# Performance work log

Hardware: AMD Instinct MI355X
Metric: run time of the kernel (lower is better)

## Reference

```python
import jax, jax.numpy as jnp
import numpy as np

EMBED = 2048
HEADS = 16
HEAD_DIM = EMBED // HEADS


def setup_inputs() -> dict:
    key = jax.random.key(0)
    k1, k2 = jax.random.split(key)
    X = jax.random.normal(k1, (2, 2048, EMBED), dtype=jnp.float32)
    W_qkv = jax.random.normal(k2, (EMBED, 3 * EMBED), dtype=jnp.float32) * (1.0 / np.sqrt(EMBED))
    b_qkv = jnp.zeros((3 * EMBED,), dtype=jnp.float32)
    return {"X": X, "W_qkv": W_qkv, "b_qkv": b_qkv}


def reference(X, W_qkv, b_qkv):
    B, S, D = X.shape
    qkv = jnp.einsum('bsd,de->bse', X, W_qkv) + b_qkv  # [B,S,3D]
    q, k, v = jnp.split(qkv, 3, axis=-1)
    # [B,S,D] -> [B,H,S,hd]
    def heads(t):
        return t.reshape(B, S, HEADS, HEAD_DIM).transpose(0, 2, 1, 3)
    q, k, v = heads(q), heads(k), heads(v)
    scale = 1.0 / np.sqrt(HEAD_DIM).astype(np.float32)
    attention_score = jnp.einsum('bhqd,bhkd->bhqk', q, k) * scale
    scores = jax.nn.softmax(attention_score, axis=-1)  # [B,H,S,S]
    attention = jnp.einsum('bhqk,bhkd->bhqd', scores, v)
    attention = attention.transpose(0, 2, 1, 3).reshape(B, S, D)
    return (attention, scores)
```

## Files before the change

### kernel.cpp

```cpp
#include <hip/hip_runtime.h>
#include <hip/hip_bf16.h>

typedef __attribute__((ext_vector_type(8))) short short8;
typedef __attribute__((ext_vector_type(4))) float floatx4;

#define SEQ 2048
#define EMB 2048
#define NH 16
#define HD 128
#define E3 6144
#define SC2 0.12751224765383853f

static __device__ __forceinline__ unsigned short f2bf(float f) {
  unsigned u = __builtin_bit_cast(unsigned, f);
  u += 0x7fffu + ((u >> 16) & 1u);
  return (unsigned short)(u >> 16);
}

__global__ void k_tw(const float* __restrict__ W, unsigned short* __restrict__ Wt) {
  __shared__ unsigned short t[32][33];
  int tx = threadIdx.x, ty = threadIdx.y;
  int e0 = blockIdx.x * 32, d0 = blockIdx.y * 32;
#pragma unroll
  for (int k = 0; k < 4; k++)
    t[ty + k * 8][tx] = f2bf(W[(long)(d0 + ty + k * 8) * E3 + e0 + tx]);
  __syncthreads();
#pragma unroll
  for (int k = 0; k < 4; k++)
    Wt[(long)(e0 + ty + k * 8) * EMB + d0 + tx] = t[tx][ty + k * 8];
}

__global__ void k_tv(const unsigned short* __restrict__ qkv, unsigned short* __restrict__ Vt) {
  __shared__ unsigned short t[32][33];
  int tx = threadIdx.x, ty = threadIdx.y;
  int z = blockIdx.z;
  int b = z >> 4, h = z & 15;
  int s0 = blockIdx.x * 32, d0 = blockIdx.y * 32;
#pragma unroll
  for (int k = 0; k < 4; k++) {
    int s = s0 + ty + k * 8;
    t[ty + k * 8][tx] = qkv[(long)(b * SEQ + s) * E3 + 2 * EMB + h * HD + d0 + tx];
  }
  __syncthreads();
#pragma unroll
  for (int k = 0; k < 4; k++) {
    int d = d0 + ty + k * 8;
    Vt[((long)z * HD + d) * SEQ + s0 + tx] = t[tx][ty + k * 8];
  }
}

template <int MODE>
__global__ __launch_bounds__(256, 2) void k_gemm(const void* __restrict__ Abase,
                                                 const unsigned short* __restrict__ Btb,
                                                 void* __restrict__ Cb,
                                                 const float* __restrict__ bias,
                                                 float scale) {
  constexpr int K = (MODE == 1) ? 128 : 2048;
  constexpr long sA = (MODE == 0) ? EMB : (MODE == 1) ? E3 : SEQ;
  constexpr long sB = (MODE == 0) ? EMB : (MODE == 1) ? E3 : SEQ;
  constexpr long sC = (MODE == 0) ? E3 : (MODE == 1) ? SEQ : EMB;
  constexpr bool AF32 = (MODE != 1);

  int z = blockIdx.z;
  long offA = 0, offB = 0, offC = 0;
  if (MODE == 1) {
    int b = z >> 4, h = z & 15;
    offA = (long)(b * SEQ) * E3 + h * HD;
    offB = (long)(b * SEQ) * E3 + EMB + h * HD;
    offC = (long)z * SEQ * SEQ;
  } else if (MODE == 2) {
    int b = z >> 4, h = z & 15;
    offA = (long)z * SEQ * SEQ;
    offB = (long)z * HD * SEQ;
    offC = (long)b * SEQ * EMB + h * HD;
  }

  __shared__ unsigned short As[128][72];
  __shared__ unsigned short Bs[128][72];

  int tid = threadIdx.x;
  int lane = tid & 63;
  int wave = tid >> 6;
  int wm = wave >> 1, wn = wave & 1;
  int quad = lane >> 4, l16 = lane & 15;
  long tM = (long)blockIdx.y * 128;
  long tN = (long)blockIdx.x * 128;

  const float* Af = (const float*)Abase;
  const unsigned short* Ab = (const unsigned short*)Abase;

  floatx4 acc[4][4] = {};

  for (int k0 = 0; k0 < K; k0 += 64) {
#pragma unroll
    for (int c = 0; c < 4; c++) {
      int id = tid + 256 * c;
      int r = id >> 3;
      int col = (id & 7) * 8;
      if (AF32) {
        const float* s = Af + offA + (tM + r) * sA + k0 + col;
        float4 f0 = *(const float4*)s;
        float4 f1 = *(const float4*)(s + 4);
        uint4 u;
        u.x = (unsigned)f2bf(f0.x) | ((unsigned)f2bf(f0.y) << 16);
        u.y = (unsigned)f2bf(f0.z) | ((unsigned)f2bf(f0.w) << 16);
        u.z = (unsigned)f2bf(f1.x) | ((unsigned)f2bf(f1.y) << 16);
        u.w = (unsigned)f2bf(f1.z) | ((unsigned)f2bf(f1.w) << 16);
        *(uint4*)&As[r][col] = u;
      } else {
        *(uint4*)&As[r][col] = *(const uint4*)(Ab + offA + (tM + r) * sA + k0 + col);
      }
      *(uint4*)&Bs[r][col] = *(const uint4*)(Btb + offB + (tN + r) * sB + k0 + col);
    }
    __syncthreads();
#pragma unroll
    for (int ks = 0; ks < 2; ks++) {
      short8 af[4], bfr[4];
#pragma unroll
      for (int i = 0; i < 4; i++)
        af[i] = *(const short8*)&As[wm * 64 + i * 16 + l16][ks * 32 + quad * 8];
#pragma unroll
      for (int j = 0; j < 4; j++)
        bfr[j] = *(const short8*)&Bs[wn * 64 + j * 16 + l16][ks * 32 + quad * 8];
#pragma unroll
      for (int i = 0; i < 4; i++)
#pragma unroll
        for (int j = 0; j < 4; j++)
          acc[i][j] = __builtin_amdgcn_mfma_f32_16x16x32_bf16(af[i], bfr[j], acc[i][j], 0, 0, 0);
    }
    __syncthreads();
  }

#pragma unroll
  for (int i = 0; i < 4; i++)
#pragma unroll
    for (int j = 0; j < 4; j++)
#pragma unroll
      for (int r = 0; r < 4; r++) {
        long row = tM + wm * 64 + i * 16 + quad * 4 + r;
        long col = tN + wn * 64 + j * 16 + l16;
        float v = acc[i][j][r];
        if (MODE == 0) {
          ((unsigned short*)Cb)[row * sC + col] = f2bf(v + bias[col]);
        } else if (MODE == 1) {
          ((float*)Cb)[offC + row * sC + col] = v * scale;
        } else {
          ((float*)Cb)[offC + row * sC + col] = v;
        }
      }
}

__global__ __launch_bounds__(256, 2) void k_attn(const unsigned short* __restrict__ qkv,
                                                 const unsigned short* __restrict__ Vt,
                                                 float* __restrict__ scores,
                                                 float* __restrict__ attn) {
  int id = blockIdx.x;
  int z = (id & 7) * 4 + ((id >> 3) >> 4);
  int qt = (id >> 3) & 15;
  int b = z >> 4, h = z & 15;

  const unsigned short* Qg = qkv + (long)b * SEQ * E3 + h * HD;
  const unsigned short* Kg = Qg + EMB;
  const unsigned short* Vg = Vt + (long)z * HD * SEQ;
  float* Sg = scores + (long)z * SEQ * SEQ + (long)qt * 128 * SEQ;
  float* Og = attn + (long)b * SEQ * EMB + (long)qt * 128 * EMB + h * HD;

  __shared__ unsigned short Kt[64][136];
  __shared__ unsigned short Vs[128][72];
  __shared__ unsigned short Ps[128][72];

  int tid = threadIdx.x;
  int lane = tid & 63, wave = tid >> 6;
  int quad = lane >> 4, l16 = lane & 15;

  short8 qf[2][4];
#pragma unroll
  for (int i = 0; i < 2; i++)
#pragma unroll
    for (int ks = 0; ks < 4; ks++)
      qf[i][ks] = *(const short8*)(Qg + (long)(qt * 128 + wave * 32 + i * 16 + l16) * E3 +
                                   ks * 32 + quad * 8);

  floatx4 oacc[2][8] = {};
  float rs[2][4] = {};

  uint4 kreg[4], vreg[4];
  auto loadK = [&](int t) {
#pragma unroll
    for (int c = 0; c < 4; c++) {
      int i2 = tid + 256 * c;
      kreg[c] = *(const uint4*)(Kg + (long)(t * 64 + (i2 >> 4)) * E3 + (i2 & 15) * 8);
    }
  };
  auto loadV = [&](int t) {
#pragma unroll
    for (int c = 0; c < 4; c++) {
      int i2 = tid + 256 * c;
      vreg[c] = *(const uint4*)(Vg + (long)(i2 >> 3) * SEQ + t * 64 + (i2 & 7) * 8);
    }
  };

  loadK(0);
  loadV(0);

  for (int t = 0; t < 32; t++) {
#pragma unroll
    for (int c = 0; c < 4; c++) {
      int i2 = tid + 256 * c;
      *(uint4*)&Kt[i2 >> 4][(i2 & 15) * 8] = kreg[c];
      *(uint4*)&Vs[i2 >> 3][(i2 & 7) * 8] = vreg[c];
    }
    __syncthreads();
    if (t < 31) { loadK(t + 1); loadV(t + 1); }

    floatx4 sacc[2][4] = {};
#pragma unroll
    for (int ks = 0; ks < 4; ks++) {
      short8 kf[4];
#pragma unroll
      for (int j = 0; j < 4; j++)
        kf[j] = *(const short8*)&Kt[j * 16 + l16][ks * 32 + quad * 8];
#pragma unroll
      for (int i = 0; i < 2; i++)
#pragma unroll
        for (int j = 0; j < 4; j++)
          sacc[i][j] = __builtin_amdgcn_mfma_f32_16x16x32_bf16(qf[i][ks], kf[j], sacc[i][j], 0, 0, 0);
    }
#pragma unroll
    for (int i = 0; i < 2; i++)
#pragma unroll
      for (int j = 0; j < 4; j++)
#pragma unroll
        for (int r = 0; r < 4; r++) {
          float e = exp2f(sacc[i][j][r] * SC2);
          rs[i][r] += e;
          Ps[wave * 32 + i * 16 + quad * 4 + r][j * 16 + l16] = f2bf(e);
        }
    __syncthreads();
#pragma unroll
    for (int ks = 0; ks < 2; ks++) {
      short8 pf[2], vf[8];
#pragma unroll
      for (int i = 0; i < 2; i++)
        pf[i] = *(const short8*)&Ps[wave * 32 + i * 16 + l16][ks * 32 + quad * 8];
#pragma unroll
      for (int j = 0; j < 8; j++)
        vf[j] = *(const short8*)&Vs[j * 16 + l16][ks * 32 + quad * 8];
#pragma unroll
      for (int i = 0; i < 2; i++)
#pragma unroll
        for (int j = 0; j < 8; j++)
          oacc[i][j] = __builtin_amdgcn_mfma_f32_16x16x32_bf16(pf[i], vf[j], oacc[i][j], 0, 0, 0);
    }
    __syncthreads();
  }

  loadK(0);

  float irs[2][4];
#pragma unroll
  for (int i = 0; i < 2; i++)
#pragma unroll
    for (int r = 0; r < 4; r++) {
      float s = rs[i][r];
      s += __shfl_xor(s, 1, 64);
      s += __shfl_xor(s, 2, 64);
      s += __shfl_xor(s, 4, 64);
      s += __shfl_xor(s, 8, 64);
      irs[i][r] = 1.0f / s;
    }

#pragma unroll
  for (int i = 0; i < 2; i++)
#pragma unroll
    for (int j = 0; j < 8; j++)
#pragma unroll
      for (int r = 0; r < 4; r++)
        Og[(long)(wave * 32 + i * 16 + quad * 4 + r) * EMB + j * 16 + l16] =
            oacc[i][j][r] * irs[i][r];

  for (int t = 0; t < 32; t++) {
#pragma unroll
    for (int c = 0; c < 4; c++) {
      int i2 = tid + 256 * c;
      *(uint4*)&Kt[i2 >> 4][(i2 & 15) * 8] = kreg[c];
    }
    __syncthreads();
    if (t < 31) loadK(t + 1);

    floatx4 sacc[2][4] = {};
#pragma unroll
    for (int ks = 0; ks < 4; ks++) {
      short8 kf[4];
#pragma unroll
      for (int j = 0; j < 4; j++)
        kf[j] = *(const short8*)&Kt[j * 16 + l16][ks * 32 + quad * 8];
#pragma unroll
      for (int i = 0; i < 2; i++)
#pragma unroll
        for (int j = 0; j < 4; j++)
          sacc[i][j] = __builtin_amdgcn_mfma_f32_16x16x32_bf16(qf[i][ks], kf[j], sacc[i][j], 0, 0, 0);
    }
#pragma unroll
    for (int i = 0; i < 2; i++)
#pragma unroll
      for (int j = 0; j < 4; j++)
#pragma unroll
        for (int r = 0; r < 4; r++)
          Sg[(long)(wave * 32 + i * 16 + quad * 4 + r) * SEQ + t * 64 + j * 16 + l16] =
              exp2f(sacc[i][j][r] * SC2) * irs[i][r];
    __syncthreads();
  }
}

extern "C" void kernel_launch(void* const* d_in, const int* in_sizes, int n_in,
                              void* d_out, int out_size, void* d_ws, size_t ws_size,
                              hipStream_t stream) {
  const float* X = (const float*)d_in[0];
  const float* W = (const float*)d_in[1];
  const float* bias = (const float*)d_in[2];
  float* out = (float*)d_out;
  float* attn = out;
  float* scores = out + (long)2 * SEQ * EMB;

  unsigned short* Wt = (unsigned short*)d_ws;
  unsigned short* qkv = Wt + (long)E3 * EMB;
  unsigned short* Vt = qkv + (long)2 * SEQ * E3;

  k_tw<<<dim3(E3 / 32, EMB / 32), dim3(32, 8), 0, stream>>>(W, Wt);
  k_gemm<0><<<dim3(E3 / 128, (2 * SEQ) / 128, 1), 256, 0, stream>>>(X, Wt, qkv, bias, 1.0f);
  k_tv<<<dim3(SEQ / 32, HD / 32, 2 * NH), dim3(32, 8), 0, stream>>>(qkv, Vt);
  k_attn<<<dim3(512), dim3(256), 0, stream>>>(qkv, Vt, scores, attn);
}
```

Baseline: 1.161 ms.

## Pre-convert X to bf16 and use direct global-to-LDS loads in projection GEMM

Adds a kernel that converts X to bf16 once, so the projection GEMM no longer converts fp32 to bf16 in every tile. The projection GEMM now fills shared memory with global_load_lds 16-byte transfers, drops the padded LDS layout, and remaps blocks with an XCD-aware swizzle. The bias is loaded once per thread into registers. The unpadded LDS layout may cause bank conflicts on fragment reads, and the new kernel adds an extra pass over X, stored in the Vt workspace before Vt is written.

Result: no change. 1.155 ms (-0.5%).

```diff
diff --git a/kernel.cpp b/kernel.cpp
--- a/kernel.cpp
+++ b/kernel.cpp
@@ -17,6 +17,24 @@
   return (unsigned short)(u >> 16);
 }
 
+static __device__ __forceinline__ void gld_lds16(const unsigned short* g, unsigned short* l) {
+  __builtin_amdgcn_global_load_lds(
+      (const __attribute__((address_space(1))) void*)g,
+      (__attribute__((address_space(3))) void*)l, 16, 0, 0);
+}
+
+__global__ void k_tx(const float* __restrict__ X, unsigned short* __restrict__ Xb) {
+  long i = ((long)blockIdx.x * 256 + threadIdx.x) * 8;
+  float4 f0 = *(const float4*)(X + i);
+  float4 f1 = *(const float4*)(X + i + 4);
+  uint4 u;
+  u.x = (unsigned)f2bf(f0.x) | ((unsigned)f2bf(f0.y) << 16);
+  u.y = (unsigned)f2bf(f0.z) | ((unsigned)f2bf(f0.w) << 16);
+  u.z = (unsigned)f2bf(f1.x) | ((unsigned)f2bf(f1.y) << 16);
+  u.w = (unsigned)f2bf(f1.z) | ((unsigned)f2bf(f1.w) << 16);
+  *(uint4*)(Xb + i) = u;
+}
+
 __global__ void k_tw(const float* __restrict__ W, unsigned short* __restrict__ Wt) {
   __shared__ unsigned short t[32][33];
   int tx = threadIdx.x, ty = threadIdx.y;
@@ -49,68 +67,32 @@
   }
 }
 
-template <int MODE>
-__global__ __launch_bounds__(256, 2) void k_gemm(const void* __restrict__ Abase,
-                                                 const unsigned short* __restrict__ Btb,
-                                                 void* __restrict__ Cb,
-                                                 const float* __restrict__ bias,
-                                                 float scale) {
-  constexpr int K = (MODE == 1) ? 128 : 2048;
-  constexpr long sA = (MODE == 0) ? EMB : (MODE == 1) ? E3 : SEQ;
-  constexpr long sB = (MODE == 0) ? EMB : (MODE == 1) ? E3 : SEQ;
-  constexpr long sC = (MODE == 0) ? E3 : (MODE == 1) ? SEQ : EMB;
-  constexpr bool AF32 = (MODE != 1);
-
-  int z = blockIdx.z;
-  long offA = 0, offB = 0, offC = 0;
-  if (MODE == 1) {
-    int b = z >> 4, h = z & 15;
-    offA = (long)(b * SEQ) * E3 + h * HD;
-    offB = (long)(b * SEQ) * E3 + EMB + h * HD;
-    offC = (long)z * SEQ * SEQ;
-  } else if (MODE == 2) {
-    int b = z >> 4, h = z & 15;
-    offA = (long)z * SEQ * SEQ;
-    offB = (long)z * HD * SEQ;
-    offC = (long)b * SEQ * EMB + h * HD;
-  }
-
-  __shared__ unsigned short As[128][72];
-  __shared__ unsigned short Bs[128][72];
-
-  int tid = threadIdx.x;
-  int lane = tid & 63;
-  int wave = tid >> 6;
-  int wm = wave >> 1, wn = wave & 1;
-  int quad = lane >> 4, l16 = lane & 15;
-  long tM = (long)blockIdx.y * 128;
-  long tN = (long)blockIdx.x * 128;
-
-  const float* Af = (const float*)Abase;
-  const unsigned short* Ab = (const unsigned short*)Abase;
+__global__ __launch_bounds__(256) void k_proj(const unsigned short* __restrict__ Xb,
+                                              const unsigned short* __restrict__ Wt,
+                                              unsigned short* __restrict__ qkv,
+                                              const float* __restrict__ bias) {
+  __shared__ unsigned short As[128][64];
+  __shared__ unsigned short Bs[128][64];
+
+  int bid = blockIdx.x;
+  int swz = (bid & 7) * 192 + (bid >> 3);
+  int bx = swz % 48, by = swz / 48;
+  long tM = (long)by * 128, tN = (long)bx * 128;
+
+  int tid = threadIdx.x, lane = tid & 63, wave = tid >> 6;
+  int wm = wave >> 1, wn = wave & 1, quad = lane >> 4, l16 = lane & 15;
+  int lr = lane >> 3, lc = (lane & 7) * 8;
+
+  const unsigned short* Ag = Xb + (tM + wave * 32 + lr) * EMB + lc;
+  const unsigned short* Bg = Wt + (tN + wave * 32 + lr) * EMB + lc;
 
   floatx4 acc[4][4] = {};
 
-  for (int k0 = 0; k0 < K; k0 += 64) {
-#pragma unroll
-    for (int c = 0; c < 4; c++) {
-      int id = tid + 256 * c;
-      int r = id >> 3;
-      int col = (id & 7) * 8;
-      if (AF32) {
-        const float* s = Af + offA + (tM + r) * sA + k0 + col;
-        float4 f0 = *(const float4*)s;
-        float4 f1 = *(const float4*)(s + 4);
-        uint4 u;
-        u.x = (unsigned)f2bf(f0.x) | ((unsigned)f2bf(f0.y) << 16);
-        u.y = (unsigned)f2bf(f0.z) | ((unsigned)f2bf(f0.w) << 16);
-        u.z = (unsigned)f2bf(f1.x) | ((unsigned)f2bf(f1.y) << 16);
-        u.w = (unsigned)f2bf(f1.z) | ((unsigned)f2bf(f1.w) << 16);
-        *(uint4*)&As[r][col] = u;
-      } else {
-        *(uint4*)&As[r][col] = *(const uint4*)(Ab + offA + (tM + r) * sA + k0 + col);
-      }
-      *(uint4*)&Bs[r][col] = *(const uint4*)(Btb + offB + (tN + r) * sB + k0 + col);
+  for (int k0 = 0; k0 < 2048; k0 += 64) {
+#pragma unroll
+    for (int c = 0; c < 4; c++) {
+      gld_lds16(Ag + (long)(c * 8) * EMB + k0, &As[wave * 32 + c * 8][0]);
+      gld_lds16(Bg + (long)(c * 8) * EMB + k0, &Bs[wave * 32 + c * 8][0]);
     }
     __syncthreads();
 #pragma unroll
@@ -130,6 +112,10 @@
     }
     __syncthreads();
   }
+
+  float b4[4];
+#pragma unroll
+  for (int j = 0; j < 4; j++) b4[j] = bias[tN + wn * 64 + j * 16 + l16];
 
 #pragma unroll
   for (int i = 0; i < 4; i++)
@@ -139,14 +125,7 @@
       for (int r = 0; r < 4; r++) {
         long row = tM + wm * 64 + i * 16 + quad * 4 + r;
         long col = tN + wn * 64 + j * 16 + l16;
-        float v = acc[i][j][r];
-        if (MODE == 0) {
-          ((unsigned short*)Cb)[row * sC + col] = f2bf(v + bias[col]);
-        } else if (MODE == 1) {
-          ((float*)Cb)[offC + row * sC + col] = v * scale;
-        } else {
-          ((float*)Cb)[offC + row * sC + col] = v;
-        }
+        qkv[row * E3 + col] = f2bf(acc[i][j][r] + b4[j]);
       }
 }
 
@@ -326,9 +305,11 @@
   unsigned short* Wt = (unsigned short*)d_ws;
   unsigned short* qkv = Wt + (long)E3 * EMB;
   unsigned short* Vt = qkv + (long)2 * SEQ * E3;
-
+  unsigned short* Xb = Vt;
+
+  k_tx<<<dim3(4096), dim3(256), 0, stream>>>(X, Xb);
   k_tw<<<dim3(E3 / 32, EMB / 32), dim3(32, 8), 0, stream>>>(W, Wt);
-  k_gemm<0><<<dim3(E3 / 128, (2 * SEQ) / 128, 1), 256, 0, stream>>>(X, Wt, qkv, bias, 1.0f);
+  k_proj<<<dim3(1536), dim3(256), 0, stream>>>(Xb, Wt, qkv, bias);
   k_tv<<<dim3(SEQ / 32, HD / 32, 2 * NH), dim3(32, 8), 0, stream>>>(qkv, Vt);
   k_attn<<<dim3(512), dim3(256), 0, stream>>>(qkv, Vt, scores, attn);
 }
```
